# Kernel tuning notes

Hardware: AMD Instinct MI355X
Metric: run time of the kernel (lower is better)

The kernel has to match this reference:

```python
import jax, jax.numpy as jnp
import numpy as np

HIDDEN = 128
SIGMA_D = 0.2
SIGMA_A = 15.0
ANGLE_K = 10
FACTOR_A = 180.0 / (SIGMA_A * np.pi)


def _div_term():
    half = HIDDEN // 2
    return jnp.exp(jnp.arange(half, dtype=jnp.float32) * (-np.log(10000.0) / half))


def _sinusoid(x):
    # x: float tensor of (integer-valued) indices; returns x.shape + (HIDDEN,)
    pos = x[..., None].astype(jnp.float32)
    dt = _div_term()
    s = jnp.sin(pos * dt)
    c = jnp.cos(pos * dt)
    # interleave: even channels sin, odd channels cos
    return jnp.stack([s, c], axis=-1).reshape(x.shape + (HIDDEN,))


def setup_inputs() -> dict:
    key = jax.random.key(0)
    k1, k2, k3, k4, k5 = jax.random.split(key, 5)
    B, N = 2, 1024
    scale = 1.0 / np.sqrt(HIDDEN)
    points = jax.random.normal(k1, (B, N, 3), dtype=jnp.float32)
    Wd = jax.random.normal(k2, (HIDDEN, HIDDEN), dtype=jnp.float32) * scale
    bd = jax.random.normal(k3, (HIDDEN,), dtype=jnp.float32) * scale
    Wa = jax.random.normal(k4, (HIDDEN, HIDDEN), dtype=jnp.float32) * scale
    ba = jax.random.normal(k5, (HIDDEN,), dtype=jnp.float32) * scale
    return {"points": points, "Wd": Wd, "bd": bd, "Wa": Wa, "ba": ba}


def _single(pts, Wd, bd, Wa, ba):
    # pts: (N, 3)
    n = pts.shape[0]
    diff = pts[:, None, :] - pts[None, :, :]            # (N, N, 3)
    dists = jnp.sqrt(jnp.sum(diff * diff, axis=-1))      # (N, N)
    idx_d = jnp.clip(jnp.round(dists / SIGMA_D), 0.0, 255.0)
    # k nearest neighbours (smallest distances, incl. self)
    _, nn = jax.lax.top_k(-dists, ANGLE_K)               # (N, K)
    vec = pts[nn] - pts[:, None, :]                      # (N, K, 3)
    vnorm = jnp.linalg.norm(vec, axis=-1, keepdims=True)
    unit = vec / (vnorm + 1e-8)
    cos_ang = jnp.clip(jnp.einsum('nkd,nld->nkl', unit, unit), -1.0, 1.0)
    angles = jnp.arccos(cos_ang)                         # (N, K, K)
    idx_a = jnp.clip(jnp.round(angles * FACTOR_A), 0.0, 255.0)
    # indices computed under no_grad in the original
    idx_d = jax.lax.stop_gradient(idx_d)
    idx_a = jax.lax.stop_gradient(idx_a)

    embed_d = _sinusoid(idx_d)                           # (N, N, C)
    embed_d = jnp.mean(embed_d @ Wd.T + bd, axis=1)      # (N, C)

    embed_a = _sinusoid(idx_a)                           # (N, K, K, C)
    embed_a = embed_a @ Wa.T + ba
    embed_a = jnp.max(embed_a.reshape(n, -1, HIDDEN), axis=1)  # (N, C)
    return embed_d + embed_a


def reference(points, Wd, bd, Wa, ba):
    return jax.vmap(_single, in_axes=(0, None, None, None, None))(points, Wd, bd, Wa, ba)
```

## Files before the change

### kernel.cpp

```cpp
#include <hip/hip_runtime.h>
#include <hip/hip_bf16.h>

#define NPTS 1024
#define HID 128
#define KNN 10
#define FLT_MAX_ 3.402823466e+38f

__global__ __launch_bounds__(512) void gse_build_tables(
    const float* __restrict__ Wd, const float* __restrict__ bd,
    const float* __restrict__ Wa, const float* __restrict__ ba,
    const float* __restrict__ pts, int nP,
    float* __restrict__ Td, float* __restrict__ Ta, float4* __restrict__ P4) {
    const int blk = blockIdx.x;
    const int tid = threadIdx.x;

    if (blk >= 272) {
        const int idx = (blk - 272) * 512 + tid;
        if (idx < nP) {
            P4[idx] = make_float4(pts[idx * 3 + 0], pts[idx * 3 + 1],
                                  pts[idx * 3 + 2], 0.0f);
        }
        return;
    }

    __shared__ float S[HID];
    __shared__ float part[512];
    const bool isA = (blk >= 256);
    const int v = isA ? blk - 256 : blk;
    const int c = tid & 127;
    const int seg = tid >> 7;

    if (tid < HID) {
        const int m = tid >> 1;
        const float dtm = expf((float)m * (float)(-9.210340371976184 / 64.0));
        const float arg = (float)v * dtm;
        S[tid] = (tid & 1) ? cosf(arg) : sinf(arg);
    }
    __syncthreads();

    const float* W = isA ? Wa : Wd;
    const float* wrow = W + c * HID + seg * 32;
    const float* srow = S + seg * 32;
    float acc = 0.0f;
    #pragma unroll
    for (int h = 0; h < 32; h += 4) {
        const float4 wv = *reinterpret_cast<const float4*>(wrow + h);
        acc += srow[h] * wv.x + srow[h + 1] * wv.y + srow[h + 2] * wv.z + srow[h + 3] * wv.w;
    }
    part[tid] = acc;
    __syncthreads();

    if (tid < HID) {
        const float s = (part[c] + part[c + 128]) + (part[c + 256] + part[c + 384]);
        if (isA) Ta[v * HID + c] = s + ba[c];
        else     Td[v * HID + c] = (s + bd[c]) * (1.0f / (float)NPTS);
    }
}

__global__ __launch_bounds__(256, 8) void gse_main(
    const float4* __restrict__ P4,
    const float* __restrict__ Td,
    const float* __restrict__ Ta,
    float* __restrict__ out) {
    const int gid = blockIdx.x;
    const int b = gid >> 10;
    const int i = gid & 1023;
    const float4* P = P4 + (size_t)b * NPTS;
    const int tid = threadIdx.x;
    const int lane = tid & 63;
    const int w = tid >> 6;

    __shared__ int h4[4][256];
    __shared__ float cd[64];
    __shared__ int cidx[64];
    __shared__ int nn[KNN];
    __shared__ float uxs[KNN], uys[KNN], uzs[KNN];
    __shared__ float sums[256], mxs[256];
    __shared__ unsigned amask_s;
    __shared__ int ccnt;

    {
        int* hf = (int*)h4;
        hf[tid] = 0; hf[tid + 256] = 0; hf[tid + 512] = 0; hf[tid + 768] = 0;
    }
    if (tid == 0) { amask_s = 0u; ccnt = 0; }
    const float4 p = P[i];
    __syncthreads();

    float d4[4];
    int q4[4];
    const int jb = w * 256;
    #pragma unroll
    for (int s = 0; s < 4; ++s) {
        const int j = jb + s * 64 + lane;
        const float4 q = P[j];
        const float dx = p.x - q.x;
        const float dy = p.y - q.y;
        const float dz = p.z - q.z;
        const float dd = sqrtf(dx * dx + dy * dy + dz * dz);
        d4[s] = dd;
        float qq = rintf(dd / 0.2f);
        qq = fminf(fmaxf(qq, 0.0f), 255.0f);
        q4[s] = (int)qq;
        atomicAdd(&h4[w][q4[s]], 1);
    }
    __syncthreads();

    const int hsum = h4[0][tid] + h4[1][tid] + h4[2][tid] + h4[3][tid];
    h4[0][tid] = hsum;
    __syncthreads();
    const int* hist = h4[0];

    int cum = hist[lane];
    #pragma unroll
    for (int off = 1; off < 64; off <<= 1) {
        const int n_ = __shfl_up(cum, off);
        if (lane >= off) cum += n_;
    }
    const unsigned long long bal = __ballot(cum >= KNN);
    const unsigned long long nz0 = __ballot(hist[lane] != 0);
    const unsigned long long nz1 = __ballot(hist[64 + lane] != 0);
    const unsigned long long nz2 = __ballot(hist[128 + lane] != 0);
    const unsigned long long nz3 = __ballot(hist[192 + lane] != 0);
    int maxbin;
    if (nz3)      maxbin = 192 + 63 - __clzll((long long)nz3);
    else if (nz2) maxbin = 128 + 63 - __clzll((long long)nz2);
    else if (nz1) maxbin = 64 + 63 - __clzll((long long)nz1);
    else          maxbin = 63 - __clzll((long long)nz0);

    int b10 = 0, c = 0;
    if (bal) { b10 = __ffsll(bal) - 1; c = __shfl(cum, b10); }
    const bool fast = (bal != 0ull) && (c <= 64);

    if (fast) {
        #pragma unroll
        for (int s = 0; s < 4; ++s) {
            if (q4[s] <= b10) {
                const int pp = atomicAdd(&ccnt, 1);
                cd[pp] = d4[s];
                cidx[pp] = jb + s * 64 + lane;
            }
        }
        __syncthreads();
        if (tid < c) {
            const float md = cd[tid];
            const int mi = cidx[tid];
            int rank = 0;
            #pragma unroll 4
            for (int pp = 0; pp < c; ++pp) {
                const float od = cd[pp];
                const int oi = cidx[pp];
                rank += (od < md || (od == md && oi < mi)) ? 1 : 0;
            }
            if (rank < KNN) nn[rank] = mi;
        }
        __syncthreads();
    } else {
        unsigned valid = 0xfu;
        float keep_d = 0.0f;
        int keep_i = 0;
        for (int r = 0; r < KNN; ++r) {
            float bv = FLT_MAX_;
            int bi = 0x7fffffff;
            #pragma unroll
            for (int s = 0; s < 4; ++s) {
                if (valid & (1u << s)) {
                    const float v_ = d4[s];
                    const int id_ = jb + s * 64 + lane;
                    if (v_ < bv || (v_ == bv && id_ < bi)) { bv = v_; bi = id_; }
                }
            }
            #pragma unroll
            for (int off = 32; off > 0; off >>= 1) {
                const float ov = __shfl_xor(bv, off);
                const int oi = __shfl_xor(bi, off);
                if (ov < bv || (ov == bv && oi < bi)) { bv = ov; bi = oi; }
            }
            const int loc = bi - jb;
            if (loc >= 0 && loc < 256 && lane == (loc & 63)) valid &= ~(1u << (loc >> 6));
            if (lane == r) { keep_d = bv; keep_i = bi; }
        }
        if (lane < KNN) { cd[w * KNN + lane] = keep_d; cidx[w * KNN + lane] = keep_i; }
        __syncthreads();
        if (tid < 4 * KNN) {
            const float md = cd[tid];
            const int mi = cidx[tid];
            int rank = 0;
            for (int pp = 0; pp < 4 * KNN; ++pp) {
                const float od = cd[pp];
                const int oi = cidx[pp];
                rank += (od < md || (od == md && oi < mi)) ? 1 : 0;
            }
            if (rank < KNN) nn[rank] = mi;
        }
        __syncthreads();
    }

    if (tid < KNN) {
        const float4 qn = P[nn[tid]];
        const float vx = qn.x - p.x;
        const float vy = qn.y - p.y;
        const float vz = qn.z - p.z;
        const float nrm = sqrtf(vx * vx + vy * vy + vz * vz);
        const float den = nrm + 1e-8f;
        uxs[tid] = vx / den; uys[tid] = vy / den; uzs[tid] = vz / den;
    }
    __syncthreads();

    if (tid < KNN * KNN) {
        const int k = tid / KNN, l = tid % KNN;
        float cc = uxs[k] * uxs[l] + uys[k] * uys[l] + uzs[k] * uzs[l];
        cc = fminf(fmaxf(cc, -1.0f), 1.0f);
        const float ang = acosf(cc);
        float q = rintf(ang * (float)(180.0 / (15.0 * M_PI)));
        q = fminf(fmaxf(q, 0.0f), 15.0f);
        atomicOr(&amask_s, 1u << (int)q);
    }
    __syncthreads();

    const unsigned am = amask_s;
    const int c7 = tid & 127;
    const int half = tid >> 7;
    float s = 0.0f;
    const float* tdc = Td + c7;
    #pragma unroll 4
    for (int v = half; v <= maxbin; v += 2) {
        s += (float)hist[v] * tdc[v * HID];
    }
    float mx = -FLT_MAX_;
    const float* tac = Ta + c7;
    #pragma unroll
    for (int v = 0; v < 8; ++v) {
        const int vv = half * 8 + v;
        const float tv = tac[vv * HID];
        if (am & (1u << vv)) mx = fmaxf(mx, tv);
    }
    sums[tid] = s;
    mxs[tid] = mx;
    __syncthreads();
    if (tid < HID) {
        out[(size_t)gid * HID + tid] =
            (sums[tid] + sums[tid + 128]) + fmaxf(mxs[tid], mxs[tid + 128]);
    }
}

extern "C" void kernel_launch(void* const* d_in, const int* in_sizes, int n_in,
                              void* d_out, int out_size, void* d_ws, size_t ws_size,
                              hipStream_t stream) {
    const float* pts = (const float*)d_in[0];
    const float* Wd  = (const float*)d_in[1];
    const float* bd  = (const float*)d_in[2];
    const float* Wa  = (const float*)d_in[3];
    const float* ba  = (const float*)d_in[4];
    float* out = (float*)d_out;

    const int B = in_sizes[0] / (NPTS * 3);
    const int nP = B * NPTS;

    float* Td = (float*)d_ws;
    float* Ta = Td + 256 * HID;
    float4* P4 = (float4*)(Ta + 16 * HID);

    const int nconv = (nP + 511) / 512;
    gse_build_tables<<<272 + nconv, 512, 0, stream>>>(Wd, bd, Wa, ba, pts, nP, Td, Ta, P4);
    gse_main<<<nP, 256, 0, stream>>>(P4, Td, Ta, out);
}
```

Measured before the change: 23.37 us.

## Assign one query point per wavefront instead of one per block

Each 64-lane wavefront now handles a whole query point on its own: it scans all 1024 candidates at 16 per lane, keeps a private histogram, compacts candidates with ballot/popcount, and combines the angle mask through shuffles. This removes the block-wide __syncthreads barriers, shared-memory atomics on counters, and cross-wave histogram merging, and it launches four times fewer blocks. The cost is higher register pressure (16 distances per lane), longer serial work per wave, and reliance on __threadfence_block in place of real barriers for intra-wave LDS visibility.

```diff
diff --git a/kernel.cpp b/kernel.cpp
--- a/kernel.cpp
+++ b/kernel.cpp
@@ -57,71 +57,62 @@
     }
 }
 
-__global__ __launch_bounds__(256, 8) void gse_main(
+__global__ __launch_bounds__(256) void gse_wave(
     const float4* __restrict__ P4,
     const float* __restrict__ Td,
     const float* __restrict__ Ta,
-    float* __restrict__ out) {
-    const int gid = blockIdx.x;
+    float* __restrict__ out, int nP) {
+    const int tid = threadIdx.x;
+    const int lane = tid & 63;
+    const int w = tid >> 6;
+    const int gid = blockIdx.x * 4 + w;
+
+    __shared__ int   hws[4][256];
+    __shared__ float cdw[4][64];
+    __shared__ int   ciw[4][64];
+    __shared__ int   nnw[4][KNN];
+
+    if (gid >= nP) return;
+
     const int b = gid >> 10;
     const int i = gid & 1023;
     const float4* P = P4 + (size_t)b * NPTS;
-    const int tid = threadIdx.x;
-    const int lane = tid & 63;
-    const int w = tid >> 6;
-
-    __shared__ int h4[4][256];
-    __shared__ float cd[64];
-    __shared__ int cidx[64];
-    __shared__ int nn[KNN];
-    __shared__ float uxs[KNN], uys[KNN], uzs[KNN];
-    __shared__ float sums[256], mxs[256];
-    __shared__ unsigned amask_s;
-    __shared__ int ccnt;
-
-    {
-        int* hf = (int*)h4;
-        hf[tid] = 0; hf[tid + 256] = 0; hf[tid + 512] = 0; hf[tid + 768] = 0;
-    }
-    if (tid == 0) { amask_s = 0u; ccnt = 0; }
     const float4 p = P[i];
-    __syncthreads();
-
-    float d4[4];
-    int q4[4];
-    const int jb = w * 256;
-    #pragma unroll
-    for (int s = 0; s < 4; ++s) {
-        const int j = jb + s * 64 + lane;
-        const float4 q = P[j];
+
+    int* H = hws[w];
+    #pragma unroll
+    for (int k = 0; k < 4; ++k) H[lane + k * 64] = 0;
+
+    float d[16];
+    unsigned pq[4];
+    #pragma unroll
+    for (int s = 0; s < 16; ++s) {
+        const float4 q = P[s * 64 + lane];
         const float dx = p.x - q.x;
         const float dy = p.y - q.y;
         const float dz = p.z - q.z;
         const float dd = sqrtf(dx * dx + dy * dy + dz * dz);
-        d4[s] = dd;
+        d[s] = dd;
         float qq = rintf(dd / 0.2f);
         qq = fminf(fmaxf(qq, 0.0f), 255.0f);
-        q4[s] = (int)qq;
-        atomicAdd(&h4[w][q4[s]], 1);
-    }
-    __syncthreads();
-
-    const int hsum = h4[0][tid] + h4[1][tid] + h4[2][tid] + h4[3][tid];
-    h4[0][tid] = hsum;
-    __syncthreads();
-    const int* hist = h4[0];
-
-    int cum = hist[lane];
+        const int qi = (int)qq;
+        if ((s & 3) == 0) pq[s >> 2] = (unsigned)qi;
+        else              pq[s >> 2] |= (unsigned)qi << ((s & 3) * 8);
+        atomicAdd(&H[qi], 1);
+    }
+    __threadfence_block();
+
+    int cum = H[lane];
     #pragma unroll
     for (int off = 1; off < 64; off <<= 1) {
         const int n_ = __shfl_up(cum, off);
         if (lane >= off) cum += n_;
     }
     const unsigned long long bal = __ballot(cum >= KNN);
-    const unsigned long long nz0 = __ballot(hist[lane] != 0);
-    const unsigned long long nz1 = __ballot(hist[64 + lane] != 0);
-    const unsigned long long nz2 = __ballot(hist[128 + lane] != 0);
-    const unsigned long long nz3 = __ballot(hist[192 + lane] != 0);
+    const unsigned long long nz0 = __ballot(H[lane] != 0);
+    const unsigned long long nz1 = __ballot(H[64 + lane] != 0);
+    const unsigned long long nz2 = __ballot(H[128 + lane] != 0);
+    const unsigned long long nz3 = __ballot(H[192 + lane] != 0);
     int maxbin;
     if (nz3)      maxbin = 192 + 63 - __clzll((long long)nz3);
     else if (nz2) maxbin = 128 + 63 - __clzll((long long)nz2);
@@ -133,40 +124,42 @@
     const bool fast = (bal != 0ull) && (c <= 64);
 
     if (fast) {
+        int base = 0;
         #pragma unroll
-        for (int s = 0; s < 4; ++s) {
-            if (q4[s] <= b10) {
-                const int pp = atomicAdd(&ccnt, 1);
-                cd[pp] = d4[s];
-                cidx[pp] = jb + s * 64 + lane;
-            }
-        }
-        __syncthreads();
-        if (tid < c) {
-            const float md = cd[tid];
-            const int mi = cidx[tid];
+        for (int s = 0; s < 16; ++s) {
+            const int qi = (int)((pq[s >> 2] >> ((s & 3) * 8)) & 255u);
+            const bool pred = (qi <= b10);
+            const unsigned long long m = __ballot(pred);
+            if (pred) {
+                const int pos = base + (int)__popcll(m & ((1ull << lane) - 1ull));
+                cdw[w][pos] = d[s];
+                ciw[w][pos] = s * 64 + lane;
+            }
+            base += (int)__popcll(m);
+        }
+        __threadfence_block();
+        if (lane < c) {
+            const float md = cdw[w][lane];
+            const int mi = ciw[w][lane];
             int rank = 0;
-            #pragma unroll 4
+            #pragma unroll 8
             for (int pp = 0; pp < c; ++pp) {
-                const float od = cd[pp];
-                const int oi = cidx[pp];
+                const float od = cdw[w][pp];
+                const int oi = ciw[w][pp];
                 rank += (od < md || (od == md && oi < mi)) ? 1 : 0;
             }
-            if (rank < KNN) nn[rank] = mi;
-        }
-        __syncthreads();
+            if (rank < KNN) nnw[w][rank] = mi;
+        }
     } else {
-        unsigned valid = 0xfu;
-        float keep_d = 0.0f;
-        int keep_i = 0;
+        unsigned valid = 0xffffu;
         for (int r = 0; r < KNN; ++r) {
             float bv = FLT_MAX_;
             int bi = 0x7fffffff;
             #pragma unroll
-            for (int s = 0; s < 4; ++s) {
+            for (int s = 0; s < 16; ++s) {
                 if (valid & (1u << s)) {
-                    const float v_ = d4[s];
-                    const int id_ = jb + s * 64 + lane;
+                    const float v_ = d[s];
+                    const int id_ = s * 64 + lane;
                     if (v_ < bv || (v_ == bv && id_ < bi)) { bv = v_; bi = id_; }
                 }
             }
@@ -176,72 +169,70 @@
                 const int oi = __shfl_xor(bi, off);
                 if (ov < bv || (ov == bv && oi < bi)) { bv = ov; bi = oi; }
             }
-            const int loc = bi - jb;
-            if (loc >= 0 && loc < 256 && lane == (loc & 63)) valid &= ~(1u << (loc >> 6));
-            if (lane == r) { keep_d = bv; keep_i = bi; }
-        }
-        if (lane < KNN) { cd[w * KNN + lane] = keep_d; cidx[w * KNN + lane] = keep_i; }
-        __syncthreads();
-        if (tid < 4 * KNN) {
-            const float md = cd[tid];
-            const int mi = cidx[tid];
-            int rank = 0;
-            for (int pp = 0; pp < 4 * KNN; ++pp) {
-                const float od = cd[pp];
-                const int oi = cidx[pp];
-                rank += (od < md || (od == md && oi < mi)) ? 1 : 0;
-            }
-            if (rank < KNN) nn[rank] = mi;
-        }
-        __syncthreads();
-    }
-
-    if (tid < KNN) {
-        const float4 qn = P[nn[tid]];
+            if (lane == (bi & 63)) valid &= ~(1u << (bi >> 6));
+            if (lane == 0) nnw[w][r] = bi;
+        }
+    }
+    __threadfence_block();
+
+    float ux = 0.0f, uy = 0.0f, uz = 0.0f;
+    if (lane < KNN) {
+        const int j = nnw[w][lane];
+        const float4 qn = P[j];
         const float vx = qn.x - p.x;
         const float vy = qn.y - p.y;
         const float vz = qn.z - p.z;
-        const float nrm = sqrtf(vx * vx + vy * vy + vz * vz);
-        const float den = nrm + 1e-8f;
-        uxs[tid] = vx / den; uys[tid] = vy / den; uzs[tid] = vz / den;
-    }
-    __syncthreads();
-
-    if (tid < KNN * KNN) {
-        const int k = tid / KNN, l = tid % KNN;
-        float cc = uxs[k] * uxs[l] + uys[k] * uys[l] + uzs[k] * uzs[l];
+        const float den = sqrtf(vx * vx + vy * vy + vz * vz) + 1e-8f;
+        ux = vx / den; uy = vy / den; uz = vz / den;
+    }
+
+    unsigned mk = 0u;
+    {
+        const int k1 = lane / 10, l1 = lane - 10 * k1;
+        const float akx = __shfl(ux, k1), aky = __shfl(uy, k1), akz = __shfl(uz, k1);
+        const float alx = __shfl(ux, l1), aly = __shfl(uy, l1), alz = __shfl(uz, l1);
+        float cc = akx * alx + aky * aly + akz * alz;
         cc = fminf(fmaxf(cc, -1.0f), 1.0f);
-        const float ang = acosf(cc);
-        float q = rintf(ang * (float)(180.0 / (15.0 * M_PI)));
+        float q = rintf(acosf(cc) * (float)(180.0 / (15.0 * M_PI)));
         q = fminf(fmaxf(q, 0.0f), 15.0f);
-        atomicOr(&amask_s, 1u << (int)q);
-    }
-    __syncthreads();
-
-    const unsigned am = amask_s;
-    const int c7 = tid & 127;
-    const int half = tid >> 7;
-    float s = 0.0f;
-    const float* tdc = Td + c7;
+        mk |= 1u << (int)q;
+    }
+    {
+        const int p2 = lane + 64;
+        const int k2 = p2 / 10, l2 = p2 - 10 * k2;
+        const int k2c = (p2 < 100) ? k2 : 0;
+        const int l2c = (p2 < 100) ? l2 : 0;
+        const float akx = __shfl(ux, k2c), aky = __shfl(uy, k2c), akz = __shfl(uz, k2c);
+        const float alx = __shfl(ux, l2c), aly = __shfl(uy, l2c), alz = __shfl(uz, l2c);
+        float cc = akx * alx + aky * aly + akz * alz;
+        cc = fminf(fmaxf(cc, -1.0f), 1.0f);
+        float q = rintf(acosf(cc) * (float)(180.0 / (15.0 * M_PI)));
+        q = fminf(fmaxf(q, 0.0f), 15.0f);
+        if (p2 < 100) mk |= 1u << (int)q;
+    }
+    #pragma unroll
+    for (int off = 32; off > 0; off >>= 1) mk |= __shfl_xor(mk, off);
+    const unsigned am = mk;
+
+    float s0 = 0.0f, s1 = 0.0f;
+    const float* tdc = Td + lane;
     #pragma unroll 4
-    for (int v = half; v <= maxbin; v += 2) {
-        s += (float)hist[v] * tdc[v * HID];
-    }
-    float mx = -FLT_MAX_;
-    const float* tac = Ta + c7;
-    #pragma unroll
-    for (int v = 0; v < 8; ++v) {
-        const int vv = half * 8 + v;
-        const float tv = tac[vv * HID];
-        if (am & (1u << vv)) mx = fmaxf(mx, tv);
-    }
-    sums[tid] = s;
-    mxs[tid] = mx;
-    __syncthreads();
-    if (tid < HID) {
-        out[(size_t)gid * HID + tid] =
-            (sums[tid] + sums[tid + 128]) + fmaxf(mxs[tid], mxs[tid + 128]);
-    }
+    for (int v = 0; v <= maxbin; ++v) {
+        const float h = (float)H[v];
+        s0 += h * tdc[v * HID];
+        s1 += h * tdc[v * HID + 64];
+    }
+    float m0 = -FLT_MAX_, m1 = -FLT_MAX_;
+    const float* tac = Ta + lane;
+    #pragma unroll
+    for (int v = 0; v < 16; ++v) {
+        const float t0 = tac[v * HID];
+        const float t1 = tac[v * HID + 64];
+        if (am & (1u << v)) { m0 = fmaxf(m0, t0); m1 = fmaxf(m1, t1); }
+    }
+    float* o = out + (size_t)gid * HID;
+    o[lane]      = s0 + m0;
+    o[lane + 64] = s1 + m1;
 }
 
 extern "C" void kernel_launch(void* const* d_in, const int* in_sizes, int n_in,
@@ -263,5 +254,5 @@
 
     const int nconv = (nP + 511) / 512;
     gse_build_tables<<<272 + nconv, 512, 0, stream>>>(Wd, bd, Wa, ba, pts, nP, Td, Ta, P4);
-    gse_main<<<nP, 256, 0, stream>>>(P4, Td, Ta, out);
+    gse_wave<<<(nP + 3) / 4, 256, 0, stream>>>(P4, Td, Ta, out, nP);
 }
```

Measured after the change: 27.36 us. +17.1%, slower.
